# Kernel optimization log

Hardware: AMD Instinct MI355X
Metric: run time of the kernel (lower is better)

Reference implementation:

```python
import jax, jax.numpy as jnp
import numpy as np

N_HEAD = 8
D_Q = 1024
D_K = 1024  # d_k_original
DK = D_K // N_HEAD  # per-head dim = 128
B = 64
L = 2048


def setup_inputs() -> dict:
    key = jax.random.key(0)
    ks = jax.random.split(key, 8)
    std_q = np.sqrt(2.0 / (D_Q + DK)).astype(np.float32)
    std_k = np.sqrt(2.0 / (D_K + DK)).astype(np.float32)
    return {
        "q": jax.random.normal(ks[0], (B, D_Q), jnp.float32),
        "k": jax.random.normal(ks[1], (B, L, D_K), jnp.float32),
        "mask": jnp.zeros((B, L), jnp.bool_),
        # Linear weights stored torch-style: (out_features, in_features)
        "w_qs_w": jax.random.normal(ks[2], (N_HEAD * DK, D_Q), jnp.float32) * std_q,
        "w_qs_b": jnp.zeros((N_HEAD * DK,), jnp.float32),
        "w_ks_w": jax.random.normal(ks[3], (N_HEAD * DK, D_K), jnp.float32) * std_k,
        "w_ks_b": jnp.zeros((N_HEAD * DK,), jnp.float32),
        "w_vs_w": jax.random.normal(ks[4], (N_HEAD * DK, D_K), jnp.float32) * std_k,
        "w_vs_b": jnp.zeros((N_HEAD * DK,), jnp.float32),
    }


def reference(q, k, mask, w_qs_w, w_qs_b, w_ks_w, w_ks_b, w_vs_w, w_vs_b):
    # Dropouts are identity (eval mode).
    b, l, _ = k.shape
    temperature = jnp.sqrt(jnp.asarray(DK, q.dtype))
    # Projections: torch Linear y = x @ W.T + b
    qs = (q @ w_qs_w.T + w_qs_b).reshape(b, N_HEAD, DK)          # (b, n, dk)
    ks = (k @ w_ks_w.T + w_ks_b).reshape(b, l, N_HEAD, DK)       # (b, l, n, dk)
    vs = (k @ w_vs_w.T + w_vs_b).reshape(b, l, N_HEAD, DK)       # (b, l, n, dv)
    # Single-query per head attention scores: (b, n, l)
    attn = jnp.einsum("bnd,blnd->bnl", qs, ks) / temperature
    attn = jnp.where(mask[:, None, :], -jnp.inf, attn)
    attn = jax.nn.softmax(attn, axis=-1)
    # Weighted sum over l: (b, n, dv) -> (b, n*dv)
    output = jnp.einsum("bnl,blnd->bnd", attn, vs).reshape(b, N_HEAD * DK)
    # attn returned head-major like original: (n*b, l)
    attn_out = attn.transpose(1, 0, 2).reshape(N_HEAD * b, l)
    return (output, attn_out)
```

## Files before the change

### kernel.cpp

```cpp
#include <hip/hip_runtime.h>
#include <hip/hip_bf16.h>
#include <math.h>

#define B 64
#define L 2048
#define C 1024
#define NH 8
#define DK 128
#define SCALE 0.08838834764831845f

__global__ void k_qs(const float* __restrict__ q, const float* __restrict__ wq,
                     const float* __restrict__ bq, float* __restrict__ qs) {
    int t = threadIdx.x, w = t >> 6, lane = t & 63;
    int j = blockIdx.x * 4 + w;
    float4 W[4];
#pragma unroll
    for (int kk = 0; kk < 4; kk++)
        W[kk] = *(const float4*)&wq[(size_t)j * C + kk * 256 + lane * 4];
    float bj = bq[j];
    for (int b = 0; b < B; b++) {
        float s = 0.f;
#pragma unroll
        for (int kk = 0; kk < 4; kk++) {
            float4 qv = *(const float4*)&q[(size_t)b * C + kk * 256 + lane * 4];
            s += W[kk].x * qv.x + W[kk].y * qv.y + W[kk].z * qv.z + W[kk].w * qv.w;
        }
#pragma unroll
        for (int off = 32; off; off >>= 1) s += __shfl_xor(s, off, 64);
        if (lane == 0) qs[(size_t)b * C + j] = s + bj;
    }
}

__global__ void k_qtilde(const float* __restrict__ qs, const float* __restrict__ wk,
                         float* __restrict__ qtilde) {
    int n = blockIdx.x >> 2, cc = blockIdx.x & 3, bg = blockIdx.y;
    int t = threadIdx.x;
    int c = cc * 256 + t;
    __shared__ float qss[8][128];
    for (int p = 0; p < 4; p++) {
        int e = p * 256 + t;
        int i = e >> 7, d = e & 127;
        qss[i][d] = qs[(size_t)(bg * 8 + i) * C + n * DK + d];
    }
    __syncthreads();
    float acc[8];
#pragma unroll
    for (int i = 0; i < 8; i++) acc[i] = 0.f;
    for (int d = 0; d < DK; d++) {
        float wv = wk[(size_t)(n * DK + d) * C + c];
#pragma unroll
        for (int i = 0; i < 8; i++) acc[i] += qss[i][d] * wv;
    }
#pragma unroll
    for (int i = 0; i < 8; i++)
        qtilde[((size_t)(bg * 8 + i) * NH + n) * C + c] = acc[i] * SCALE;
}

__global__ __launch_bounds__(512, 2) void k_fused3(
    const float* __restrict__ kmat, const float* __restrict__ qtilde,
    const unsigned char* __restrict__ mask,
    float* __restrict__ pout,
    float* __restrict__ accpart,
    float* __restrict__ zpart) {
    const int b = blockIdx.x, lp = blockIdx.y;
    const int t = threadIdx.x, w = t >> 6, lane = t & 63;
    const int chunk = w >> 1;
    const int hg = w & 1;
    const int l0 = lp * 512 + chunk * 128;
    const int hl = lane & 3;

    __shared__ float ctxl[NH * C];
    __shared__ float zl[NH];

    float4 qt[4][4];
#pragma unroll
    for (int j = 0; j < 4; j++)
#pragma unroll
        for (int kk = 0; kk < 4; kk++)
            qt[j][kk] = *(const float4*)&qtilde[((size_t)b * NH + hg * 4 + j) * C + kk * 256 + lane * 4];

    float4 acc[4][4];
#pragma unroll
    for (int j = 0; j < 4; j++)
#pragma unroll
        for (int kk = 0; kk < 4; kk++) acc[j][kk] = make_float4(0.f, 0.f, 0.f, 0.f);
    float zacc = 0.f;

    const float* kp = kmat + ((size_t)b * L + l0) * C + lane * 4;
    const unsigned char* mp = mask + (size_t)b * L + l0;

    float4 kv[2][4];
#pragma unroll
    for (int kk = 0; kk < 4; kk++) kv[0][kk] = *(const float4*)(kp + kk * 256);

    for (int rb = 0; rb < 32; rb++) {
        uchar4 mb = *(const uchar4*)&mp[rb * 4];
        float ss[4];
#pragma unroll
        for (int rr = 0; rr < 4; rr++) {
            const int r = rb * 4 + rr;
            const int cur = r & 1;
            if (r < 127) {
                const float* np = kp + (size_t)(r + 1) * C;
#pragma unroll
                for (int kk = 0; kk < 4; kk++)
                    kv[cur ^ 1][kk] = *(const float4*)(np + kk * 256);
            }
            float s0 = 0.f, s1 = 0.f, s2 = 0.f, s3 = 0.f;
#pragma unroll
            for (int kk = 0; kk < 4; kk++) {
                float4 kq = kv[cur][kk];
                s0 += qt[0][kk].x * kq.x + qt[0][kk].y * kq.y + qt[0][kk].z * kq.z + qt[0][kk].w * kq.w;
                s1 += qt[1][kk].x * kq.x + qt[1][kk].y * kq.y + qt[1][kk].z * kq.z + qt[1][kk].w * kq.w;
                s2 += qt[2][kk].x * kq.x + qt[2][kk].y * kq.y + qt[2][kk].z * kq.z + qt[2][kk].w * kq.w;
                s3 += qt[3][kk].x * kq.x + qt[3][kk].y * kq.y + qt[3][kk].z * kq.z + qt[3][kk].w * kq.w;
            }
            float a01 = (lane & 1) ? s1 : s0;
            float g01 = (lane & 1) ? s0 : s1;
            float a23 = (lane & 1) ? s3 : s2;
            float g23 = (lane & 1) ? s2 : s3;
            float u  = a01 + __shfl_xor(g01, 1, 64);
            float v2 = a23 + __shfl_xor(g23, 1, 64);
            float keep = (lane & 2) ? v2 : u;
            float give = (lane & 2) ? u : v2;
            float v = keep + __shfl_xor(give, 2, 64);
            v += __shfl_xor(v, 4, 64);
            v += __shfl_xor(v, 8, 64);
            v += __shfl_xor(v, 16, 64);
            v += __shfl_xor(v, 32, 64);
            unsigned char mk = (rr == 0) ? mb.x : (rr == 1) ? mb.y : (rr == 2) ? mb.z : mb.w;
            float p = __expf(mk ? -INFINITY : v);
            zacc += p;
            ss[rr] = p;
            float p1 = __shfl_xor(p, 1, 64);
            float p2 = __shfl_xor(p, 2, 64);
            float p3 = __shfl_xor(p1, 2, 64);
#pragma unroll
            for (int kk = 0; kk < 4; kk++) {
                float4 kq = kv[cur][kk];
                acc[0][kk].x += p  * kq.x; acc[0][kk].y += p  * kq.y; acc[0][kk].z += p  * kq.z; acc[0][kk].w += p  * kq.w;
                acc[1][kk].x += p1 * kq.x; acc[1][kk].y += p1 * kq.y; acc[1][kk].z += p1 * kq.z; acc[1][kk].w += p1 * kq.w;
                acc[2][kk].x += p2 * kq.x; acc[2][kk].y += p2 * kq.y; acc[2][kk].z += p2 * kq.z; acc[2][kk].w += p2 * kq.w;
                acc[3][kk].x += p3 * kq.x; acc[3][kk].y += p3 * kq.y; acc[3][kk].z += p3 * kq.z; acc[3][kk].w += p3 * kq.w;
            }
        }
        if (lane < 4) {
            float4 o = make_float4(ss[0], ss[1], ss[2], ss[3]);
            *(float4*)&pout[((size_t)(hg * 4 + lane) * B + b) * L + l0 + rb * 4] = o;
        }
    }

    __syncthreads();
    for (int ph = 0; ph < 4; ph++) {
        if (chunk == ph) {
#pragma unroll
            for (int j = 0; j < 4; j++) {
                int h = hg * 4 + (hl ^ j);
                float* dst = &ctxl[(size_t)h * C + lane * 4];
                if (ph == 0) {
#pragma unroll
                    for (int kk = 0; kk < 4; kk++)
                        *(float4*)&dst[kk * 256] = acc[j][kk];
                } else {
#pragma unroll
                    for (int kk = 0; kk < 4; kk++) {
                        float4 o = *(const float4*)&dst[kk * 256];
                        float4 a = acc[j][kk];
                        o.x += a.x; o.y += a.y; o.z += a.z; o.w += a.w;
                        *(float4*)&dst[kk * 256] = o;
                    }
                }
            }
            if (lane < 4) {
                if (ph == 0) zl[hg * 4 + lane] = zacc;
                else         zl[hg * 4 + lane] += zacc;
            }
        }
        __syncthreads();
    }
    float* ap = accpart + ((size_t)b * 4 + lp) * (NH * C);
#pragma unroll
    for (int i = 0; i < 4; i++) {
        int idx = t * 16 + i * 4;
        *(float4*)&ap[idx] = *(const float4*)&ctxl[idx];
    }
    if (t < NH) zpart[((size_t)b * 4 + lp) * NH + t] = zl[t];
}

__global__ void k_combine(const float* __restrict__ accpart, const float* __restrict__ zpart,
                          float* __restrict__ ctx, float* __restrict__ Zinv) {
    int b = blockIdx.x, cq = blockIdx.y;
    int t = threadIdx.x;
    int c = cq * 256 + t;
    __shared__ float zi[NH];
    if (t < NH) {
        float z = 0.f;
#pragma unroll
        for (int lpp = 0; lpp < 4; lpp++) z += zpart[((size_t)b * 4 + lpp) * NH + t];
        float inv = 1.0f / z;
        zi[t] = inv;
        if (cq == 0) Zinv[t * B + b] = inv;
    }
    __syncthreads();
#pragma unroll
    for (int n = 0; n < NH; n++) {
        float s = 0.f;
#pragma unroll
        for (int lpp = 0; lpp < 4; lpp++)
            s += accpart[(((size_t)b * 4 + lpp) * NH + n) * C + c];
        ctx[((size_t)b * NH + n) * C + c] = s * zi[n];
    }
}

__global__ void k_attnnorm(float* __restrict__ attn, const float* __restrict__ Zinv) {
    int row = blockIdx.x;
    int t = threadIdx.x;
    float Zi = Zinv[row];
    float* p = attn + (size_t)row * L;
#pragma unroll
    for (int j = 0; j < 2; j++) {
        int pos = j * 1024 + t * 4;
        float4 s = *(const float4*)&p[pos];
        s.x *= Zi; s.y *= Zi; s.z *= Zi; s.w *= Zi;
        *(float4*)&p[pos] = s;
    }
}

__global__ void k_out(const float* __restrict__ ctx, const float* __restrict__ wv,
                      const float* __restrict__ bv, float* __restrict__ out) {
    int t = threadIdx.x, w = t >> 6, lane = t & 63;
    int j = blockIdx.x * 4 + w;
    int n = j >> 7;
    float4 W[4];
#pragma unroll
    for (int kk = 0; kk < 4; kk++)
        W[kk] = *(const float4*)&wv[(size_t)j * C + kk * 256 + lane * 4];
    float bj = bv[j];
    for (int b = 0; b < B; b++) {
        float s = 0.f;
#pragma unroll
        for (int kk = 0; kk < 4; kk++) {
            float4 cv = *(const float4*)&ctx[((size_t)b * NH + n) * C + kk * 256 + lane * 4];
            s += W[kk].x * cv.x + W[kk].y * cv.y + W[kk].z * cv.z + W[kk].w * cv.w;
        }
#pragma unroll
        for (int off = 32; off; off >>= 1) s += __shfl_xor(s, off, 64);
        if (lane == 0) out[(size_t)b * (NH * DK) + j] = s + bj;
    }
}

extern "C" void kernel_launch(void* const* d_in, const int* in_sizes, int n_in,
                              void* d_out, int out_size, void* d_ws, size_t ws_size,
                              hipStream_t stream) {
    const float* q    = (const float*)d_in[0];
    const float* kmat = (const float*)d_in[1];
    const unsigned char* mask = (const unsigned char*)d_in[2];
    const float* wq = (const float*)d_in[3];
    const float* bq = (const float*)d_in[4];
    const float* wk = (const float*)d_in[5];
    const float* wv = (const float*)d_in[7];
    const float* bv = (const float*)d_in[8];

    float* out  = (float*)d_out;
    float* attn = out + B * NH * DK;

    float* ws      = (float*)d_ws;
    float* qs      = ws;
    float* zpart   = ws;
    float* Zinv    = ws + 2048;
    float* qtilde  = ws + 65536;
    float* ctx     = qtilde;
    float* accpart = ws + 65536 + 524288;

    hipLaunchKernelGGL(k_qs, dim3(256), dim3(256), 0, stream, q, wq, bq, qs);
    hipLaunchKernelGGL(k_qtilde, dim3(32, 8), dim3(256), 0, stream, qs, wk, qtilde);
    hipLaunchKernelGGL(k_fused3, dim3(64, 4), dim3(512), 0, stream,
                       kmat, qtilde, mask, attn, accpart, zpart);
    hipLaunchKernelGGL(k_combine, dim3(64, 4), dim3(256), 0, stream,
                       accpart, zpart, ctx, Zinv);
    hipLaunchKernelGGL(k_attnnorm, dim3(512), dim3(256), 0, stream, attn, Zinv);
    hipLaunchKernelGGL(k_out, dim3(256), dim3(256), 0, stream, ctx, wv, bv, out);
}
```

Baseline: 243.6 us.

## Fuse combine, attention normalization and output projection into one epilogue kernel

Replaces the combine, attention-normalize and output-projection kernels with a single per-batch epilogue kernel. It reduces the partial accumulators into shared memory, runs the Wv projection from shared memory, and rescales the attention rows in place. This removes two kernel launches and the global ctx/Zinv round trip. In exchange, every block rereads the whole Wv matrix and only 64 blocks run, which lowers parallelism on a 256-CU device.

```diff
diff --git a/kernel.cpp b/kernel.cpp
--- a/kernel.cpp
+++ b/kernel.cpp
@@ -187,65 +187,62 @@
     if (t < NH) zpart[((size_t)b * 4 + lp) * NH + t] = zl[t];
 }
 
-__global__ void k_combine(const float* __restrict__ accpart, const float* __restrict__ zpart,
-                          float* __restrict__ ctx, float* __restrict__ Zinv) {
-    int b = blockIdx.x, cq = blockIdx.y;
-    int t = threadIdx.x;
-    int c = cq * 256 + t;
+__global__ __launch_bounds__(1024) void k_epilogue(
+    const float* __restrict__ accpart, const float* __restrict__ zpart,
+    const float* __restrict__ wvw, const float* __restrict__ bv,
+    float* __restrict__ pout, float* __restrict__ out) {
+    const int b = blockIdx.x;
+    const int t = threadIdx.x;
+    __shared__ float ctxl[NH * C];
     __shared__ float zi[NH];
     if (t < NH) {
         float z = 0.f;
 #pragma unroll
-        for (int lpp = 0; lpp < 4; lpp++) z += zpart[((size_t)b * 4 + lpp) * NH + t];
-        float inv = 1.0f / z;
-        zi[t] = inv;
-        if (cq == 0) Zinv[t * B + b] = inv;
-    }
-    __syncthreads();
-#pragma unroll
-    for (int n = 0; n < NH; n++) {
-        float s = 0.f;
-#pragma unroll
-        for (int lpp = 0; lpp < 4; lpp++)
-            s += accpart[(((size_t)b * 4 + lpp) * NH + n) * C + c];
-        ctx[((size_t)b * NH + n) * C + c] = s * zi[n];
-    }
-}
-
-__global__ void k_attnnorm(float* __restrict__ attn, const float* __restrict__ Zinv) {
-    int row = blockIdx.x;
-    int t = threadIdx.x;
-    float Zi = Zinv[row];
-    float* p = attn + (size_t)row * L;
-#pragma unroll
-    for (int j = 0; j < 2; j++) {
-        int pos = j * 1024 + t * 4;
-        float4 s = *(const float4*)&p[pos];
-        s.x *= Zi; s.y *= Zi; s.z *= Zi; s.w *= Zi;
-        *(float4*)&p[pos] = s;
-    }
-}
-
-__global__ void k_out(const float* __restrict__ ctx, const float* __restrict__ wv,
-                      const float* __restrict__ bv, float* __restrict__ out) {
-    int t = threadIdx.x, w = t >> 6, lane = t & 63;
-    int j = blockIdx.x * 4 + w;
-    int n = j >> 7;
-    float4 W[4];
-#pragma unroll
-    for (int kk = 0; kk < 4; kk++)
-        W[kk] = *(const float4*)&wv[(size_t)j * C + kk * 256 + lane * 4];
-    float bj = bv[j];
-    for (int b = 0; b < B; b++) {
-        float s = 0.f;
-#pragma unroll
-        for (int kk = 0; kk < 4; kk++) {
-            float4 cv = *(const float4*)&ctx[((size_t)b * NH + n) * C + kk * 256 + lane * 4];
-            s += W[kk].x * cv.x + W[kk].y * cv.y + W[kk].z * cv.z + W[kk].w * cv.w;
-        }
-#pragma unroll
-        for (int off = 32; off; off >>= 1) s += __shfl_xor(s, off, 64);
-        if (lane == 0) out[(size_t)b * (NH * DK) + j] = s + bj;
+        for (int lp = 0; lp < 4; lp++) z += zpart[((size_t)b * 4 + lp) * NH + t];
+        zi[t] = 1.0f / z;
+    }
+    __syncthreads();
+#pragma unroll
+    for (int i = 0; i < 2; i++) {
+        int f4 = i * 1024 + t;
+        float4 s = make_float4(0.f, 0.f, 0.f, 0.f);
+#pragma unroll
+        for (int lp = 0; lp < 4; lp++) {
+            float4 a = *(const float4*)&accpart[((size_t)b * 4 + lp) * (NH * C) + f4 * 4];
+            s.x += a.x; s.y += a.y; s.z += a.z; s.w += a.w;
+        }
+        float sc = zi[f4 >> 8];
+        s.x *= sc; s.y *= sc; s.z *= sc; s.w *= sc;
+        *(float4*)&ctxl[f4 * 4] = s;
+    }
+    __syncthreads();
+    {
+        int wv_i = t >> 6, lane = t & 63;
+        for (int jj = 0; jj < 64; jj++) {
+            int j = wv_i * 64 + jj;
+            int n = j >> 7;
+            float s = 0.f;
+#pragma unroll
+            for (int kk = 0; kk < 4; kk++) {
+                float4 W = *(const float4*)&wvw[(size_t)j * C + kk * 256 + lane * 4];
+                float4 cv = *(const float4*)&ctxl[(size_t)n * C + kk * 256 + lane * 4];
+                s += W.x * cv.x + W.y * cv.y + W.z * cv.z + W.w * cv.w;
+            }
+#pragma unroll
+            for (int off = 32; off; off >>= 1) s += __shfl_xor(s, off, 64);
+            if (lane == 0) out[(size_t)b * (NH * DK) + j] = s + bv[j];
+        }
+    }
+    float4* p4 = (float4*)pout;
+#pragma unroll
+    for (int i = 0; i < 4; i++) {
+        int e = i * 1024 + t;
+        int n = e >> 9, off = e & 511;
+        size_t idx = ((size_t)n * B + b) * (L / 4) + off;
+        float4 v = p4[idx];
+        float sc = zi[n];
+        v.x *= sc; v.y *= sc; v.z *= sc; v.w *= sc;
+        p4[idx] = v;
     }
 }
 
@@ -267,17 +264,13 @@
     float* ws      = (float*)d_ws;
     float* qs      = ws;
     float* zpart   = ws;
-    float* Zinv    = ws + 2048;
     float* qtilde  = ws + 65536;
-    float* ctx     = qtilde;
     float* accpart = ws + 65536 + 524288;
 
     hipLaunchKernelGGL(k_qs, dim3(256), dim3(256), 0, stream, q, wq, bq, qs);
     hipLaunchKernelGGL(k_qtilde, dim3(32, 8), dim3(256), 0, stream, qs, wk, qtilde);
     hipLaunchKernelGGL(k_fused3, dim3(64, 4), dim3(512), 0, stream,
                        kmat, qtilde, mask, attn, accpart, zpart);
-    hipLaunchKernelGGL(k_combine, dim3(64, 4), dim3(256), 0, stream,
-                       accpart, zpart, ctx, Zinv);
-    hipLaunchKernelGGL(k_attnnorm, dim3(512), dim3(256), 0, stream, attn, Zinv);
-    hipLaunchKernelGGL(k_out, dim3(256), dim3(256), 0, stream, ctx, wv, bv, out);
-}
+    hipLaunchKernelGGL(k_epilogue, dim3(64), dim3(1024), 0, stream,
+                       accpart, zpart, wv, bv, attn, out);
+}
```

Result: slower. 270.6 us (+11.1%).
